# Optimization experiments

Measured on AMD Instinct MI355X. Metric: run time of the kernel, lower is better.

Reference implementation:

```python
import jax, jax.numpy as jnp
import numpy as np

D_MODEL = 1024
N_HEAD = 16
D_HEAD = 64


def setup_inputs() -> dict:
    key = jax.random.key(0)
    k1, k2, k3 = jax.random.split(key, 3)
    B, T = 2, 2048
    x = jax.random.normal(k1, (B, T, D_MODEL), dtype=jnp.float32)
    # Linear weights (scaled like typical init to keep softmax numerics sane)
    w_attn = jax.random.normal(k2, (D_MODEL, 3 * D_MODEL), dtype=jnp.float32) * (1.0 / np.sqrt(D_MODEL))
    w_proj = jax.random.normal(k3, (D_MODEL, D_MODEL), dtype=jnp.float32) * (1.0 / np.sqrt(D_MODEL))
    return {"x": x, "w_attn": w_attn, "w_proj": w_proj}


def reference(x, w_attn, w_proj):
    B, T, C = x.shape
    # c_attn: fused qkv projection (use_bias=False)
    qkv = jnp.einsum('btc,cf->btf', x, w_attn)  # [B, T, 3C]
    q, k, v = jnp.split(qkv, 3, axis=-1)
    q = q.reshape(B, T, N_HEAD, D_HEAD)
    k = k.reshape(B, T, N_HEAD, D_HEAD)
    v = v.reshape(B, T, N_HEAD, D_HEAD)
    # scaled QK^T with causal mask (cache=None training path)
    att = jnp.einsum('bqhd,bkhd->bhqk', q, k) * (1.0 / jnp.sqrt(jnp.float32(D_HEAD)))
    causal = jnp.tril(jnp.ones((T, T), dtype=bool))  # [T, T]
    att = jnp.where(causal[None, None, :, :], att, -jnp.inf)
    att = jax.nn.softmax(att, axis=-1)
    # dropout is a no-op (deterministic / p=0)
    y = jnp.einsum('bhqk,bkhd->bqhd', att, v).reshape(B, T, C)
    y = jnp.einsum('btc,cd->btd', y, w_proj)
    return y
```

## Files before the change

kernel.cpp:

```cpp
#include <hip/hip_runtime.h>
#include <hip/hip_bf16.h>


typedef __attribute__((ext_vector_type(8))) __bf16 bf16x8;
typedef __attribute__((ext_vector_type(4))) float  floatx4;
typedef __attribute__((ext_vector_type(4))) float  fvec4;
typedef __attribute__((ext_vector_type(4))) short  short4v;

#define MFMA16(a, b, c) __builtin_amdgcn_mfma_f32_16x16x32_bf16(a, b, c, 0, 0, 0)

using as1v = const __attribute__((address_space(1))) void;
using as3v = __attribute__((address_space(3))) void;
__device__ __forceinline__ void async16(const void* g, void* l) {
  __builtin_amdgcn_global_load_lds((as1v*)g, (as3v*)l, 16, 0, 0);
}

__global__ __launch_bounds__(256) void prep_kernel(const float* __restrict__ x,
                                                   const float* __restrict__ w_attn,
                                                   const float* __restrict__ w_proj,
                                                   __hip_bfloat16* __restrict__ xb,
                                                   __hip_bfloat16* __restrict__ wat,
                                                   __hip_bfloat16* __restrict__ wpt) {
  const int bid = blockIdx.x, tid = threadIdx.x;
  if (bid < 4096) {
    const int i = (bid * 256 + tid) * 4;
    fvec4 v = *(const fvec4*)(x + i);
    union { short4v s; __hip_bfloat16 h[4]; } u;
#pragma unroll
    for (int j = 0; j < 4; ++j) u.h[j] = __float2bfloat16(v[j]);
    *(short4v*)((short*)xb + i) = u.s;
    return;
  }
  __shared__ __align__(16) __hip_bfloat16 tile[64 * 64];
  const float* in;
  __hip_bfloat16* out;
  int cols, bx, by;
  if (bid < 4864) {
    const int b2 = bid - 4096;
    in = w_attn; out = wat; cols = 3072; bx = b2 % 48; by = b2 / 48;
  } else {
    const int b2 = bid - 4864;
    in = w_proj; out = wpt; cols = 1024; bx = b2 % 16; by = b2 / 16;
  }
  const int c0 = bx * 64, r0 = by * 64;
#pragma unroll
  for (int it = 0; it < 2; ++it) {
    const int c = it * 256 + tid;
    const int row = c >> 3, cg = c & 7;
    const float* src = in + (long)(r0 + row) * cols + c0 + cg * 8;
    fvec4 v0 = *(const fvec4*)src;
    fvec4 v1 = *(const fvec4*)(src + 4);
    union { bf16x8 v; __hip_bfloat16 h[8]; } u;
#pragma unroll
    for (int j = 0; j < 4; ++j) { u.h[j] = __float2bfloat16(v0[j]); u.h[4 + j] = __float2bfloat16(v1[j]); }
    *(bf16x8*)(tile + row * 64 + (cg ^ ((row >> 3) & 7)) * 8) = u.v;
  }
  __syncthreads();
#pragma unroll
  for (int it = 0; it < 2; ++it) {
    const int c = it * 256 + tid;
    const int dr = c >> 3, tg = c & 7;
    union { bf16x8 v; __hip_bfloat16 e[8]; } u;
    const int pg = (dr >> 3) ^ tg;
#pragma unroll
    for (int j = 0; j < 8; ++j)
      u.e[j] = tile[(tg * 8 + j) * 64 + pg * 8 + (dr & 7)];
    *(bf16x8*)(out + (long)(c0 + dr) * 1024 + r0 + tg * 8) = u.v;
  }
}

__global__ __launch_bounds__(256) void gemm_qkv_kernel(const __hip_bfloat16* __restrict__ A,
                                                       const __hip_bfloat16* __restrict__ Bt,
                                                       __hip_bfloat16* __restrict__ qk,
                                                       __hip_bfloat16* __restrict__ vt,
                                                       float qscale) {
  const int K = 1024;
  __shared__ __align__(16) __hip_bfloat16 As[2][128 * 32];
  __shared__ __align__(16) __hip_bfloat16 Bs[2][128 * 32];
  const int tid = threadIdx.x;
  const int lane = tid & 63, wv = tid >> 6;
  const int l15 = lane & 15, quad = lane >> 4;
  const int wm = wv >> 1, wn = wv & 1;
  const long m0 = (long)blockIdx.y * 128, n0 = (long)blockIdx.x * 128;
  floatx4 acc[4][4] = {};
  const int nk = K >> 5;

  auto issue = [&](int kt, int p) {
    const int k0 = kt << 5;
#pragma unroll
    for (int it = 0; it < 2; ++it) {
      const int c = it * 256 + tid;
      const int row = c >> 2;
      const int lcg = (c & 3) ^ ((row >> 1) & 3);
      async16(A + (m0 + row) * K + k0 + lcg * 8, (char*)&As[p][0] + c * 16);
      async16(Bt + (n0 + row) * K + k0 + lcg * 8, (char*)&Bs[p][0] + c * 16);
    }
  };

  issue(0, 0);
  for (int kt = 0; kt < nk; ++kt) {
    const int p = kt & 1;
    __syncthreads();
    if (kt + 1 < nk) issue(kt + 1, p ^ 1);
    bf16x8 af[4], bfr[4];
#pragma unroll
    for (int t = 0; t < 4; ++t) {
      const int ar = wm * 64 + t * 16 + l15;
      const int br = wn * 64 + t * 16 + l15;
      af[t]  = *(const bf16x8*)(&As[p][ar * 32 + (quad ^ ((ar >> 1) & 3)) * 8]);
      bfr[t] = *(const bf16x8*)(&Bs[p][br * 32 + (quad ^ ((br >> 1) & 3)) * 8]);
    }
#pragma unroll
    for (int mt = 0; mt < 4; ++mt)
#pragma unroll
      for (int nt = 0; nt < 4; ++nt)
        acc[mt][nt] = MFMA16(af[mt], bfr[nt], acc[mt][nt]);
  }

#pragma unroll
  for (int nt = 0; nt < 4; ++nt) {
    const int colb = (int)n0 + wn * 64 + nt * 16;
    if (colb >= 2048) {
      const int hh = (colb - 2048) >> 6;
      const int d  = (colb & 63) + l15;
#pragma unroll
      for (int mt = 0; mt < 4; ++mt) {
        const long row = m0 + wm * 64 + mt * 16 + quad * 4;
        const long b   = row >> 11;
        const long t0  = row & 2047;
        union { short4v s; __hip_bfloat16 h[4]; } uy;
#pragma unroll
        for (int r = 0; r < 4; ++r) uy.h[r] = __float2bfloat16(acc[mt][nt][r]);
        *(short4v*)(vt + ((b * 16 + hh) * 64 + d) * 2048 + t0) = uy.s;
      }
    } else {
      const float sc = (colb < 1024) ? qscale : 1.0f;
      const long col = colb + l15;
#pragma unroll
      for (int mt = 0; mt < 4; ++mt)
#pragma unroll
        for (int r = 0; r < 4; ++r) {
          const long row = m0 + wm * 64 + mt * 16 + quad * 4 + r;
          qk[row * 2048 + col] = __float2bfloat16(acc[mt][nt][r] * sc);
        }
    }
  }
}

__global__ __launch_bounds__(256) void gemm_bt128_kernel(const __hip_bfloat16* __restrict__ A,
                                                         const __hip_bfloat16* __restrict__ Bt,
                                                         float* __restrict__ C,
                                                         int M, int N, int K) {
  __shared__ __align__(16) __hip_bfloat16 As[2][128 * 32];
  __shared__ __align__(16) __hip_bfloat16 Bs[2][128 * 32];
  const int tid = threadIdx.x;
  const int lane = tid & 63, wv = tid >> 6;
  const int l15 = lane & 15, quad = lane >> 4;
  const int wm = wv >> 1, wn = wv & 1;
  const long m0 = (long)blockIdx.y * 128, n0 = (long)blockIdx.x * 128;
  floatx4 acc[4][4] = {};
  const int nk = K >> 5;

  auto issue = [&](int kt, int p) {
    const int k0 = kt << 5;
#pragma unroll
    for (int it = 0; it < 2; ++it) {
      const int c = it * 256 + tid;
      const int row = c >> 2;
      const int lcg = (c & 3) ^ ((row >> 1) & 3);
      async16(A + (m0 + row) * K + k0 + lcg * 8, (char*)&As[p][0] + c * 16);
      async16(Bt + (n0 + row) * K + k0 + lcg * 8, (char*)&Bs[p][0] + c * 16);
    }
  };

  issue(0, 0);
  for (int kt = 0; kt < nk; ++kt) {
    const int p = kt & 1;
    __syncthreads();
    if (kt + 1 < nk) issue(kt + 1, p ^ 1);
    bf16x8 af[4], bfr[4];
#pragma unroll
    for (int t = 0; t < 4; ++t) {
      const int ar = wm * 64 + t * 16 + l15;
      const int br = wn * 64 + t * 16 + l15;
      af[t]  = *(const bf16x8*)(&As[p][ar * 32 + (quad ^ ((ar >> 1) & 3)) * 8]);
      bfr[t] = *(const bf16x8*)(&Bs[p][br * 32 + (quad ^ ((br >> 1) & 3)) * 8]);
    }
#pragma unroll
    for (int mt = 0; mt < 4; ++mt)
#pragma unroll
      for (int nt = 0; nt < 4; ++nt)
        acc[mt][nt] = MFMA16(af[mt], bfr[nt], acc[mt][nt]);
  }
#pragma unroll
  for (int mt = 0; mt < 4; ++mt)
#pragma unroll
    for (int nt = 0; nt < 4; ++nt)
#pragma unroll
      for (int r = 0; r < 4; ++r) {
        const long row = m0 + wm * 64 + mt * 16 + quad * 4 + r;
        const long col = n0 + wn * 64 + nt * 16 + l15;
        C[row * N + col] = acc[mt][nt][r];
      }
}

__global__ __launch_bounds__(512, 2) void attn_kernel(const __hip_bfloat16* __restrict__ qk,
                                                      const __hip_bfloat16* __restrict__ vtg,
                                                      __hip_bfloat16* __restrict__ y) {
  __shared__ __align__(16) char smem[81920];
  __hip_bfloat16* KsB = (__hip_bfloat16*)smem;
  __hip_bfloat16* VtB = (__hip_bfloat16*)(smem + 32768);
  __hip_bfloat16* PbB = (__hip_bfloat16*)(smem + 65536);

  const int tid = threadIdx.x;
  const int lane = tid & 63, wv = tid >> 6;
  const int l15 = lane & 15, quad = lane >> 4;
  const int g = wv >> 2, sub = wv & 3;
  const int wg = blockIdx.x;
  const int xcd = wg & 7;
  const int r_ = wg >> 3;
  const int pt = r_ & 15;
  const int hb = xcd + 8 * (r_ >> 4);
  const int h = hb & 15, b = hb >> 4;
  const int qtA = pt, qtB = 31 - pt;
  const int q0A = qtA * 64, q0B = qtB * 64;
  const long bh = (long)b * 16 + h;
  const long RS = 2048;

  const int srow = tid >> 3;
  const int scg = (tid & 7) ^ (srow & 7);
  const __hip_bfloat16* kbase = qk + ((long)b * 2048 + srow) * RS + 1024 + h * 64 + scg * 8;
  const __hip_bfloat16* vbase = vtg + (bh * 64 + srow) * 2048 + scg * 8;
  char* ldst = smem + tid * 16;

  auto issue = [&](int pr, int buf) {
#pragma unroll
    for (int par = 0; par < 2; ++par) {
      const int kt = 2 * pr + par;
      if (kt <= qtB) {
        const long kb = (long)kt * 64;
        async16(kbase + kb * RS, ldst + buf * 16384 + par * 8192);
        async16(vbase + kb,      ldst + 32768 + buf * 16384 + par * 8192);
      }
    }
  };

  bf16x8 bqA0, bqA1, bqB0, bqB1;
  {
    const __hip_bfloat16* qpA = qk + ((long)b * 2048 + q0A + sub * 16 + l15) * RS + h * 64 + quad * 8;
    bqA0 = *(const bf16x8*)qpA;
    bqA1 = *(const bf16x8*)(qpA + 32);
    const __hip_bfloat16* qpB = qk + ((long)b * 2048 + q0B + sub * 16 + l15) * RS + h * 64 + quad * 8;
    bqB0 = *(const bf16x8*)qpB;
    bqB1 = *(const bf16x8*)(qpB + 32);
  }
  union { bf16x8 v; __hip_bfloat16 e[8]; } uo;
#pragma unroll
  for (int j = 0; j < 8; ++j) uo.e[j] = __float2bfloat16(1.0f);
  const bf16x8 ones = uo.v;

  floatx4 oA[4] = {}, oB[4] = {}, o4A = {}, o4B = {};
  __hip_bfloat16* Pw = PbB + wv * (16 * 64);
  const int m7 = l15 & 7;

  const int npairs = (qtB + 2) >> 1;
  issue(0, 0);
  for (int pr = 0; pr < npairs; ++pr) {
    const int buf = pr & 1;
    __syncthreads();
    if (pr + 1 < npairs) issue(pr + 1, buf ^ 1);
    const int kt = 2 * pr + g;
    if (kt > qtB) continue;
    const int kb = kt * 64;
    const __hip_bfloat16* Ksp = KsB + buf * 8192 + g * 4096;
    const __hip_bfloat16* Vsp = VtB + buf * 8192 + g * 4096;

    bf16x8 kf[4][2], vf[4][2];
#pragma unroll
    for (int nt = 0; nt < 4; ++nt) {
      const int row = nt * 16 + l15;
      const int s0 = (quad ^ (row & 7)) * 8, s1 = ((quad + 4) ^ (row & 7)) * 8;
      kf[nt][0] = *(const bf16x8*)(Ksp + row * 64 + s0);
      kf[nt][1] = *(const bf16x8*)(Ksp + row * 64 + s1);
      vf[nt][0] = *(const bf16x8*)(Vsp + row * 64 + s0);
      vf[nt][1] = *(const bf16x8*)(Vsp + row * 64 + s1);
    }

    auto tile = [&](const bf16x8& bq0, const bf16x8& bq1, floatx4* o, floatx4& o4,
                    bool diag, int q0X) {
      floatx4 st[4] = {};
#pragma unroll
      for (int nt = 0; nt < 4; ++nt) {
        st[nt] = MFMA16(kf[nt][0], bq0, st[nt]);
        st[nt] = MFMA16(kf[nt][1], bq1, st[nt]);
      }
      if (diag) {
        const int qg = q0X + sub * 16 + l15;
#pragma unroll
        for (int nt = 0; nt < 4; ++nt) {
          union { short4v s; __hip_bfloat16 h[4]; } up;
#pragma unroll
          for (int r = 0; r < 4; ++r) {
            float pv = exp2f(st[nt][r]);
            if (kb + nt * 16 + quad * 4 + r > qg) pv = 0.f;
            up.h[r] = __float2bfloat16(pv);
          }
          const int chunk = (nt * 2 + (quad >> 1)) ^ m7;
          *(short4v*)(Pw + l15 * 64 + chunk * 8 + (quad & 1) * 4) = up.s;
        }
      } else {
#pragma unroll
        for (int nt = 0; nt < 4; ++nt) {
          union { short4v s; __hip_bfloat16 h[4]; } up;
#pragma unroll
          for (int r = 0; r < 4; ++r) up.h[r] = __float2bfloat16(exp2f(st[nt][r]));
          const int chunk = (nt * 2 + (quad >> 1)) ^ m7;
          *(short4v*)(Pw + l15 * 64 + chunk * 8 + (quad & 1) * 4) = up.s;
        }
      }
      const bf16x8 pb0 = *(const bf16x8*)(Pw + l15 * 64 + (quad ^ m7) * 8);
      const bf16x8 pb1 = *(const bf16x8*)(Pw + l15 * 64 + ((quad + 4) ^ m7) * 8);
#pragma unroll
      for (int mt = 0; mt < 4; ++mt) {
        o[mt] = MFMA16(vf[mt][0], pb0, o[mt]);
        o[mt] = MFMA16(vf[mt][1], pb1, o[mt]);
      }
      o4 = MFMA16(ones, pb0, o4);
      o4 = MFMA16(ones, pb1, o4);
    };

    tile(bqB0, bqB1, oB, o4B, kt == qtB, q0B);
    if (kt <= qtA) tile(bqA0, bqA1, oA, o4A, kt == qtA, q0A);
  }

  __syncthreads();
  floatx4* redv = (floatx4*)smem;
  if (g == 1) {
#pragma unroll
    for (int mt = 0; mt < 4; ++mt) {
      redv[(sub * 10 + mt) * 64 + lane] = oA[mt];
      redv[(sub * 10 + 4 + mt) * 64 + lane] = oB[mt];
    }
    redv[(sub * 10 + 8) * 64 + lane] = o4A;
    redv[(sub * 10 + 9) * 64 + lane] = o4B;
  }
  __syncthreads();
  if (g == 0) {
#pragma unroll
    for (int mt = 0; mt < 4; ++mt) {
      oA[mt] += redv[(sub * 10 + mt) * 64 + lane];
      oB[mt] += redv[(sub * 10 + 4 + mt) * 64 + lane];
    }
    o4A += redv[(sub * 10 + 8) * 64 + lane];
    o4B += redv[(sub * 10 + 9) * 64 + lane];

    auto epi = [&](floatx4* o, floatx4& o4, int q0X) {
      const float inv = 1.0f / o4[0];
      const long t = (long)b * 2048 + q0X + sub * 16 + l15;
#pragma unroll
      for (int mt = 0; mt < 4; ++mt) {
        union { short4v s; __hip_bfloat16 h[4]; } uy;
#pragma unroll
        for (int r = 0; r < 4; ++r) uy.h[r] = __float2bfloat16(o[mt][r] * inv);
        *(short4v*)(y + t * 1024 + h * 64 + mt * 16 + quad * 4) = uy.s;
      }
    };
    epi(oA, o4A, q0A);
    epi(oB, o4B, q0B);
  }
}

extern "C" void kernel_launch(void* const* d_in, const int* in_sizes, int n_in,
                              void* d_out, int out_size, void* d_ws, size_t ws_size,
                              hipStream_t stream) {
  const float* x      = (const float*)d_in[0];
  const float* w_attn = (const float*)d_in[1];
  const float* w_proj = (const float*)d_in[2];
  float* out = (float*)d_out;
  char* ws = (char*)d_ws;
  __hip_bfloat16* xb  = (__hip_bfloat16*)(ws);
  __hip_bfloat16* wat = (__hip_bfloat16*)(ws + 8388608);
  __hip_bfloat16* qk  = (__hip_bfloat16*)(ws + 16777216);
  __hip_bfloat16* wpt = (__hip_bfloat16*)(ws + 33554432);
  __hip_bfloat16* vtg = (__hip_bfloat16*)(ws + 35651584);
  __hip_bfloat16* yb  = wat;
  const float SC = 0.18033688011112042f;

  prep_kernel<<<5120, 256, 0, stream>>>(x, w_attn, w_proj, xb, wat, wpt);
  gemm_qkv_kernel<<<dim3(24, 32), 256, 0, stream>>>(xb, wat, qk, vtg, SC);
  attn_kernel<<<512, 512, 0, stream>>>(qk, vtg, yb);
  gemm_bt128_kernel<<<dim3(8, 32), 256, 0, stream>>>(yb, wpt, out, 4096, 1024, 1024);
}
```

Baseline: 182.1 us.

## Compute softmax row sums in fp32 and interleave the two query tiles' stages

Drops the extra MFMA with an all-ones operand that produced the softmax denominator. Each lane now accumulates the exp values in fp32 and the partial sums are combined with cross-lane shuffles and an LDS reduction. The per-tile lambda is also split up so the QK MFMAs for tile A are issued while tile B's probabilities are written to LDS, and the V fragment loads are deferred. This removes two MFMAs per tile and gives more room for overlap, but it adds VALU adds, shuffles and some register pressure. The denominator now comes from unrounded fp32 values rather than the bf16-rounded ones.

```diff
diff --git a/kernel.cpp b/kernel.cpp
--- a/kernel.cpp
+++ b/kernel.cpp
@@ -254,12 +254,9 @@
     bqB0 = *(const bf16x8*)qpB;
     bqB1 = *(const bf16x8*)(qpB + 32);
   }
-  union { bf16x8 v; __hip_bfloat16 e[8]; } uo;
-#pragma unroll
-  for (int j = 0; j < 8; ++j) uo.e[j] = __float2bfloat16(1.0f);
-  const bf16x8 ones = uo.v;
-
-  floatx4 oA[4] = {}, oB[4] = {}, o4A = {}, o4B = {};
+
+  floatx4 oA[4] = {}, oB[4] = {};
+  float dsA = 0.f, dsB = 0.f;
   __hip_bfloat16* Pw = PbB + wv * (16 * 64);
   const int m7 = l15 & 7;
 
@@ -272,101 +269,139 @@
     const int kt = 2 * pr + g;
     if (kt > qtB) continue;
     const int kb = kt * 64;
+    const bool actA = (kt <= qtA);
     const __hip_bfloat16* Ksp = KsB + buf * 8192 + g * 4096;
     const __hip_bfloat16* Vsp = VtB + buf * 8192 + g * 4096;
 
-    bf16x8 kf[4][2], vf[4][2];
+    auto storeP = [&](floatx4* st, bool diag, int q0X, float& ds) {
+      if (diag) {
+        const int qg = q0X + sub * 16 + l15;
+#pragma unroll
+        for (int nt = 0; nt < 4; ++nt) {
+          union { short4v s; __hip_bfloat16 h2[4]; } up;
+#pragma unroll
+          for (int r = 0; r < 4; ++r) {
+            float pv = exp2f(st[nt][r]);
+            if (kb + nt * 16 + quad * 4 + r > qg) pv = 0.f;
+            ds += pv;
+            up.h2[r] = __float2bfloat16(pv);
+          }
+          const int chunk = (nt * 2 + (quad >> 1)) ^ m7;
+          *(short4v*)(Pw + l15 * 64 + chunk * 8 + (quad & 1) * 4) = up.s;
+        }
+      } else {
+#pragma unroll
+        for (int nt = 0; nt < 4; ++nt) {
+          union { short4v s; __hip_bfloat16 h2[4]; } up;
+#pragma unroll
+          for (int r = 0; r < 4; ++r) {
+            float pv = exp2f(st[nt][r]);
+            ds += pv;
+            up.h2[r] = __float2bfloat16(pv);
+          }
+          const int chunk = (nt * 2 + (quad >> 1)) ^ m7;
+          *(short4v*)(Pw + l15 * 64 + chunk * 8 + (quad & 1) * 4) = up.s;
+        }
+      }
+    };
+
+    bf16x8 kf[4][2];
 #pragma unroll
     for (int nt = 0; nt < 4; ++nt) {
       const int row = nt * 16 + l15;
       const int s0 = (quad ^ (row & 7)) * 8, s1 = ((quad + 4) ^ (row & 7)) * 8;
       kf[nt][0] = *(const bf16x8*)(Ksp + row * 64 + s0);
       kf[nt][1] = *(const bf16x8*)(Ksp + row * 64 + s1);
+    }
+
+    floatx4 st[4] = {};
+#pragma unroll
+    for (int nt = 0; nt < 4; ++nt) {
+      st[nt] = MFMA16(kf[nt][0], bqB0, st[nt]);
+      st[nt] = MFMA16(kf[nt][1], bqB1, st[nt]);
+    }
+    storeP(st, kt == qtB, q0B, dsB);
+
+    if (actA) {
+#pragma unroll
+      for (int nt = 0; nt < 4; ++nt) {
+        floatx4 z = {};
+        z = MFMA16(kf[nt][0], bqA0, z);
+        z = MFMA16(kf[nt][1], bqA1, z);
+        st[nt] = z;
+      }
+    }
+    const bf16x8 pbB0 = *(const bf16x8*)(Pw + l15 * 64 + (quad ^ m7) * 8);
+    const bf16x8 pbB1 = *(const bf16x8*)(Pw + l15 * 64 + ((quad + 4) ^ m7) * 8);
+    if (actA) storeP(st, kt == qtA, q0A, dsA);
+
+    bf16x8 vf[4][2];
+#pragma unroll
+    for (int nt = 0; nt < 4; ++nt) {
+      const int row = nt * 16 + l15;
+      const int s0 = (quad ^ (row & 7)) * 8, s1 = ((quad + 4) ^ (row & 7)) * 8;
       vf[nt][0] = *(const bf16x8*)(Vsp + row * 64 + s0);
       vf[nt][1] = *(const bf16x8*)(Vsp + row * 64 + s1);
     }
-
-    auto tile = [&](const bf16x8& bq0, const bf16x8& bq1, floatx4* o, floatx4& o4,
-                    bool diag, int q0X) {
-      floatx4 st[4] = {};
-#pragma unroll
-      for (int nt = 0; nt < 4; ++nt) {
-        st[nt] = MFMA16(kf[nt][0], bq0, st[nt]);
-        st[nt] = MFMA16(kf[nt][1], bq1, st[nt]);
-      }
-      if (diag) {
-        const int qg = q0X + sub * 16 + l15;
-#pragma unroll
-        for (int nt = 0; nt < 4; ++nt) {
-          union { short4v s; __hip_bfloat16 h[4]; } up;
-#pragma unroll
-          for (int r = 0; r < 4; ++r) {
-            float pv = exp2f(st[nt][r]);
-            if (kb + nt * 16 + quad * 4 + r > qg) pv = 0.f;
-            up.h[r] = __float2bfloat16(pv);
-          }
-          const int chunk = (nt * 2 + (quad >> 1)) ^ m7;
-          *(short4v*)(Pw + l15 * 64 + chunk * 8 + (quad & 1) * 4) = up.s;
-        }
-      } else {
-#pragma unroll
-        for (int nt = 0; nt < 4; ++nt) {
-          union { short4v s; __hip_bfloat16 h[4]; } up;
-#pragma unroll
-          for (int r = 0; r < 4; ++r) up.h[r] = __float2bfloat16(exp2f(st[nt][r]));
-          const int chunk = (nt * 2 + (quad >> 1)) ^ m7;
-          *(short4v*)(Pw + l15 * 64 + chunk * 8 + (quad & 1) * 4) = up.s;
-        }
-      }
-      const bf16x8 pb0 = *(const bf16x8*)(Pw + l15 * 64 + (quad ^ m7) * 8);
-      const bf16x8 pb1 = *(const bf16x8*)(Pw + l15 * 64 + ((quad + 4) ^ m7) * 8);
+    bf16x8 pbA0 = pbB0, pbA1 = pbB1;
+    if (actA) {
+      pbA0 = *(const bf16x8*)(Pw + l15 * 64 + (quad ^ m7) * 8);
+      pbA1 = *(const bf16x8*)(Pw + l15 * 64 + ((quad + 4) ^ m7) * 8);
+    }
+#pragma unroll
+    for (int mt = 0; mt < 4; ++mt) {
+      oB[mt] = MFMA16(vf[mt][0], pbB0, oB[mt]);
+      oB[mt] = MFMA16(vf[mt][1], pbB1, oB[mt]);
+    }
+    if (actA) {
 #pragma unroll
       for (int mt = 0; mt < 4; ++mt) {
-        o[mt] = MFMA16(vf[mt][0], pb0, o[mt]);
-        o[mt] = MFMA16(vf[mt][1], pb1, o[mt]);
-      }
-      o4 = MFMA16(ones, pb0, o4);
-      o4 = MFMA16(ones, pb1, o4);
-    };
-
-    tile(bqB0, bqB1, oB, o4B, kt == qtB, q0B);
-    if (kt <= qtA) tile(bqA0, bqA1, oA, o4A, kt == qtA, q0A);
-  }
+        oA[mt] = MFMA16(vf[mt][0], pbA0, oA[mt]);
+        oA[mt] = MFMA16(vf[mt][1], pbA1, oA[mt]);
+      }
+    }
+  }
+
+  dsA += __shfl_xor(dsA, 16, 64);
+  dsA += __shfl_xor(dsA, 32, 64);
+  dsB += __shfl_xor(dsB, 16, 64);
+  dsB += __shfl_xor(dsB, 32, 64);
 
   __syncthreads();
   floatx4* redv = (floatx4*)smem;
+  float*   redd = (float*)(smem + 32768);
   if (g == 1) {
 #pragma unroll
     for (int mt = 0; mt < 4; ++mt) {
-      redv[(sub * 10 + mt) * 64 + lane] = oA[mt];
-      redv[(sub * 10 + 4 + mt) * 64 + lane] = oB[mt];
-    }
-    redv[(sub * 10 + 8) * 64 + lane] = o4A;
-    redv[(sub * 10 + 9) * 64 + lane] = o4B;
+      redv[(sub * 8 + mt) * 64 + lane] = oA[mt];
+      redv[(sub * 8 + 4 + mt) * 64 + lane] = oB[mt];
+    }
+    redd[(sub * 2 + 0) * 64 + lane] = dsA;
+    redd[(sub * 2 + 1) * 64 + lane] = dsB;
   }
   __syncthreads();
   if (g == 0) {
 #pragma unroll
     for (int mt = 0; mt < 4; ++mt) {
-      oA[mt] += redv[(sub * 10 + mt) * 64 + lane];
-      oB[mt] += redv[(sub * 10 + 4 + mt) * 64 + lane];
-    }
-    o4A += redv[(sub * 10 + 8) * 64 + lane];
-    o4B += redv[(sub * 10 + 9) * 64 + lane];
-
-    auto epi = [&](floatx4* o, floatx4& o4, int q0X) {
-      const float inv = 1.0f / o4[0];
+      oA[mt] += redv[(sub * 8 + mt) * 64 + lane];
+      oB[mt] += redv[(sub * 8 + 4 + mt) * 64 + lane];
+    }
+    dsA += redd[(sub * 2 + 0) * 64 + lane];
+    dsB += redd[(sub * 2 + 1) * 64 + lane];
+
+    auto epi = [&](floatx4* o, float ds, int q0X) {
+      const float inv = 1.0f / ds;
       const long t = (long)b * 2048 + q0X + sub * 16 + l15;
 #pragma unroll
       for (int mt = 0; mt < 4; ++mt) {
-        union { short4v s; __hip_bfloat16 h[4]; } uy;
-#pragma unroll
-        for (int r = 0; r < 4; ++r) uy.h[r] = __float2bfloat16(o[mt][r] * inv);
+        union { short4v s; __hip_bfloat16 h2[4]; } uy;
+#pragma unroll
+        for (int r = 0; r < 4; ++r) uy.h2[r] = __float2bfloat16(o[mt][r] * inv);
         *(short4v*)(y + t * 1024 + h * 64 + mt * 16 + quad * 4) = uy.s;
       }
     };
-    epi(oA, o4A, q0A);
-    epi(oB, o4B, q0B);
+    epi(oA, dsA, q0A);
+    epi(oB, dsB, q0B);
   }
 }
 
```

Measured after the change: 184.6 us. No clear change (+1.4%).

## Load K/V directly from global per wave, drop LDS staging and split-K reduction

Applied to the files above, without the earlier changes.

The attention kernel no longer stages K and V tiles through double-buffered LDS with async loads. Each wave now reads its K and V fragments straight from global memory, and the two wave groups each own one query tile instead of splitting keys and reducing through shared memory. The softmax denominator now comes from a shuffle-reduced scalar sum rather than extra MFMAs against a ones vector. This removes barriers, the reduction pass and LDS traffic, but K/V reuse across waves now depends on cache hits, and waves in the same block do unbalanced amounts of work (pt versus 31-pt tiles).

```diff
diff --git a/kernel.cpp b/kernel.cpp
--- a/kernel.cpp
+++ b/kernel.cpp
@@ -207,166 +207,112 @@
 __global__ __launch_bounds__(512, 2) void attn_kernel(const __hip_bfloat16* __restrict__ qk,
                                                       const __hip_bfloat16* __restrict__ vtg,
                                                       __hip_bfloat16* __restrict__ y) {
-  __shared__ __align__(16) char smem[81920];
-  __hip_bfloat16* KsB = (__hip_bfloat16*)smem;
-  __hip_bfloat16* VtB = (__hip_bfloat16*)(smem + 32768);
-  __hip_bfloat16* PbB = (__hip_bfloat16*)(smem + 65536);
+  __shared__ __align__(16) __hip_bfloat16 Pb[8][16 * 64];
 
   const int tid = threadIdx.x;
   const int lane = tid & 63, wv = tid >> 6;
   const int l15 = lane & 15, quad = lane >> 4;
-  const int g = wv >> 2, sub = wv & 3;
+  const int sub = wv & 3;
   const int wg = blockIdx.x;
   const int xcd = wg & 7;
   const int r_ = wg >> 3;
   const int pt = r_ & 15;
   const int hb = xcd + 8 * (r_ >> 4);
   const int h = hb & 15, b = hb >> 4;
-  const int qtA = pt, qtB = 31 - pt;
-  const int q0A = qtA * 64, q0B = qtB * 64;
+  const int qt = (wv >> 2) ? (31 - pt) : pt;
+  const int q0 = qt * 64;
   const long bh = (long)b * 16 + h;
   const long RS = 2048;
 
-  const int srow = tid >> 3;
-  const int scg = (tid & 7) ^ (srow & 7);
-  const __hip_bfloat16* kbase = qk + ((long)b * 2048 + srow) * RS + 1024 + h * 64 + scg * 8;
-  const __hip_bfloat16* vbase = vtg + (bh * 64 + srow) * 2048 + scg * 8;
-  char* ldst = smem + tid * 16;
-
-  auto issue = [&](int pr, int buf) {
-#pragma unroll
-    for (int par = 0; par < 2; ++par) {
-      const int kt = 2 * pr + par;
-      if (kt <= qtB) {
-        const long kb = (long)kt * 64;
-        async16(kbase + kb * RS, ldst + buf * 16384 + par * 8192);
-        async16(vbase + kb,      ldst + 32768 + buf * 16384 + par * 8192);
+  bf16x8 bq0, bq1;
+  {
+    const __hip_bfloat16* qp = qk + ((long)b * 2048 + q0 + sub * 16 + l15) * RS + h * 64 + quad * 8;
+    bq0 = *(const bf16x8*)qp;
+    bq1 = *(const bf16x8*)(qp + 32);
+  }
+
+  const __hip_bfloat16* kp[4];
+  const __hip_bfloat16* vp[4];
+#pragma unroll
+  for (int nt = 0; nt < 4; ++nt) {
+    kp[nt] = qk + ((long)b * 2048 + nt * 16 + l15) * RS + 1024 + h * 64 + quad * 8;
+    vp[nt] = vtg + (bh * 64 + nt * 16 + l15) * RS + quad * 8;
+  }
+
+  floatx4 o[4] = {};
+  float ds = 0.f;
+  __hip_bfloat16* Pw = &Pb[wv][0];
+  const int m7 = l15 & 7;
+
+  for (int kt = 0; kt <= qt; ++kt) {
+    const int kb = kt * 64;
+    const long koff = (long)kb * RS;
+    bf16x8 fr[4][2];
+#pragma unroll
+    for (int nt = 0; nt < 4; ++nt) {
+      fr[nt][0] = *(const bf16x8*)(kp[nt] + koff);
+      fr[nt][1] = *(const bf16x8*)(kp[nt] + koff + 32);
+    }
+    floatx4 st[4] = {};
+#pragma unroll
+    for (int nt = 0; nt < 4; ++nt) {
+      st[nt] = MFMA16(fr[nt][0], bq0, st[nt]);
+      st[nt] = MFMA16(fr[nt][1], bq1, st[nt]);
+    }
+    if (kt == qt) {
+      const int qg = q0 + sub * 16 + l15;
+#pragma unroll
+      for (int nt = 0; nt < 4; ++nt) {
+        union { short4v s; __hip_bfloat16 h2[4]; } up;
+#pragma unroll
+        for (int r = 0; r < 4; ++r) {
+          float pv = exp2f(st[nt][r]);
+          if (kb + nt * 16 + quad * 4 + r > qg) pv = 0.f;
+          ds += pv;
+          up.h2[r] = __float2bfloat16(pv);
+        }
+        const int chunk = (nt * 2 + (quad >> 1)) ^ m7;
+        *(short4v*)(Pw + l15 * 64 + chunk * 8 + (quad & 1) * 4) = up.s;
       }
-    }
-  };
-
-  bf16x8 bqA0, bqA1, bqB0, bqB1;
-  {
-    const __hip_bfloat16* qpA = qk + ((long)b * 2048 + q0A + sub * 16 + l15) * RS + h * 64 + quad * 8;
-    bqA0 = *(const bf16x8*)qpA;
-    bqA1 = *(const bf16x8*)(qpA + 32);
-    const __hip_bfloat16* qpB = qk + ((long)b * 2048 + q0B + sub * 16 + l15) * RS + h * 64 + quad * 8;
-    bqB0 = *(const bf16x8*)qpB;
-    bqB1 = *(const bf16x8*)(qpB + 32);
-  }
-  union { bf16x8 v; __hip_bfloat16 e[8]; } uo;
-#pragma unroll
-  for (int j = 0; j < 8; ++j) uo.e[j] = __float2bfloat16(1.0f);
-  const bf16x8 ones = uo.v;
-
-  floatx4 oA[4] = {}, oB[4] = {}, o4A = {}, o4B = {};
-  __hip_bfloat16* Pw = PbB + wv * (16 * 64);
-  const int m7 = l15 & 7;
-
-  const int npairs = (qtB + 2) >> 1;
-  issue(0, 0);
-  for (int pr = 0; pr < npairs; ++pr) {
-    const int buf = pr & 1;
-    __syncthreads();
-    if (pr + 1 < npairs) issue(pr + 1, buf ^ 1);
-    const int kt = 2 * pr + g;
-    if (kt > qtB) continue;
-    const int kb = kt * 64;
-    const __hip_bfloat16* Ksp = KsB + buf * 8192 + g * 4096;
-    const __hip_bfloat16* Vsp = VtB + buf * 8192 + g * 4096;
-
-    bf16x8 kf[4][2], vf[4][2];
+    } else {
+#pragma unroll
+      for (int nt = 0; nt < 4; ++nt) {
+        union { short4v s; __hip_bfloat16 h2[4]; } up;
+#pragma unroll
+        for (int r = 0; r < 4; ++r) {
+          float pv = exp2f(st[nt][r]);
+          ds += pv;
+          up.h2[r] = __float2bfloat16(pv);
+        }
+        const int chunk = (nt * 2 + (quad >> 1)) ^ m7;
+        *(short4v*)(Pw + l15 * 64 + chunk * 8 + (quad & 1) * 4) = up.s;
+      }
+    }
+    const bf16x8 pb0 = *(const bf16x8*)(Pw + l15 * 64 + (quad ^ m7) * 8);
+    const bf16x8 pb1 = *(const bf16x8*)(Pw + l15 * 64 + ((quad + 4) ^ m7) * 8);
 #pragma unroll
     for (int nt = 0; nt < 4; ++nt) {
-      const int row = nt * 16 + l15;
-      const int s0 = (quad ^ (row & 7)) * 8, s1 = ((quad + 4) ^ (row & 7)) * 8;
-      kf[nt][0] = *(const bf16x8*)(Ksp + row * 64 + s0);
-      kf[nt][1] = *(const bf16x8*)(Ksp + row * 64 + s1);
-      vf[nt][0] = *(const bf16x8*)(Vsp + row * 64 + s0);
-      vf[nt][1] = *(const bf16x8*)(Vsp + row * 64 + s1);
-    }
-
-    auto tile = [&](const bf16x8& bq0, const bf16x8& bq1, floatx4* o, floatx4& o4,
-                    bool diag, int q0X) {
-      floatx4 st[4] = {};
-#pragma unroll
-      for (int nt = 0; nt < 4; ++nt) {
-        st[nt] = MFMA16(kf[nt][0], bq0, st[nt]);
-        st[nt] = MFMA16(kf[nt][1], bq1, st[nt]);
-      }
-      if (diag) {
-        const int qg = q0X + sub * 16 + l15;
-#pragma unroll
-        for (int nt = 0; nt < 4; ++nt) {
-          union { short4v s; __hip_bfloat16 h[4]; } up;
-#pragma unroll
-          for (int r = 0; r < 4; ++r) {
-            float pv = exp2f(st[nt][r]);
-            if (kb + nt * 16 + quad * 4 + r > qg) pv = 0.f;
-            up.h[r] = __float2bfloat16(pv);
-          }
-          const int chunk = (nt * 2 + (quad >> 1)) ^ m7;
-          *(short4v*)(Pw + l15 * 64 + chunk * 8 + (quad & 1) * 4) = up.s;
-        }
-      } else {
-#pragma unroll
-        for (int nt = 0; nt < 4; ++nt) {
-          union { short4v s; __hip_bfloat16 h[4]; } up;
-#pragma unroll
-          for (int r = 0; r < 4; ++r) up.h[r] = __float2bfloat16(exp2f(st[nt][r]));
-          const int chunk = (nt * 2 + (quad >> 1)) ^ m7;
-          *(short4v*)(Pw + l15 * 64 + chunk * 8 + (quad & 1) * 4) = up.s;
-        }
-      }
-      const bf16x8 pb0 = *(const bf16x8*)(Pw + l15 * 64 + (quad ^ m7) * 8);
-      const bf16x8 pb1 = *(const bf16x8*)(Pw + l15 * 64 + ((quad + 4) ^ m7) * 8);
-#pragma unroll
-      for (int mt = 0; mt < 4; ++mt) {
-        o[mt] = MFMA16(vf[mt][0], pb0, o[mt]);
-        o[mt] = MFMA16(vf[mt][1], pb1, o[mt]);
-      }
-      o4 = MFMA16(ones, pb0, o4);
-      o4 = MFMA16(ones, pb1, o4);
-    };
-
-    tile(bqB0, bqB1, oB, o4B, kt == qtB, q0B);
-    if (kt <= qtA) tile(bqA0, bqA1, oA, o4A, kt == qtA, q0A);
-  }
-
-  __syncthreads();
-  floatx4* redv = (floatx4*)smem;
-  if (g == 1) {
+      fr[nt][0] = *(const bf16x8*)(vp[nt] + kb);
+      fr[nt][1] = *(const bf16x8*)(vp[nt] + kb + 32);
+    }
 #pragma unroll
     for (int mt = 0; mt < 4; ++mt) {
-      redv[(sub * 10 + mt) * 64 + lane] = oA[mt];
-      redv[(sub * 10 + 4 + mt) * 64 + lane] = oB[mt];
-    }
-    redv[(sub * 10 + 8) * 64 + lane] = o4A;
-    redv[(sub * 10 + 9) * 64 + lane] = o4B;
-  }
-  __syncthreads();
-  if (g == 0) {
-#pragma unroll
-    for (int mt = 0; mt < 4; ++mt) {
-      oA[mt] += redv[(sub * 10 + mt) * 64 + lane];
-      oB[mt] += redv[(sub * 10 + 4 + mt) * 64 + lane];
-    }
-    o4A += redv[(sub * 10 + 8) * 64 + lane];
-    o4B += redv[(sub * 10 + 9) * 64 + lane];
-
-    auto epi = [&](floatx4* o, floatx4& o4, int q0X) {
-      const float inv = 1.0f / o4[0];
-      const long t = (long)b * 2048 + q0X + sub * 16 + l15;
-#pragma unroll
-      for (int mt = 0; mt < 4; ++mt) {
-        union { short4v s; __hip_bfloat16 h[4]; } uy;
-#pragma unroll
-        for (int r = 0; r < 4; ++r) uy.h[r] = __float2bfloat16(o[mt][r] * inv);
-        *(short4v*)(y + t * 1024 + h * 64 + mt * 16 + quad * 4) = uy.s;
-      }
-    };
-    epi(oA, o4A, q0A);
-    epi(oB, o4B, q0B);
+      o[mt] = MFMA16(fr[mt][0], pb0, o[mt]);
+      o[mt] = MFMA16(fr[mt][1], pb1, o[mt]);
+    }
+  }
+
+  ds += __shfl_xor(ds, 16, 64);
+  ds += __shfl_xor(ds, 32, 64);
+  const float inv = 1.0f / ds;
+
+  const long t = (long)b * 2048 + q0 + sub * 16 + l15;
+#pragma unroll
+  for (int mt = 0; mt < 4; ++mt) {
+    union { short4v s; __hip_bfloat16 h2[4]; } uy;
+#pragma unroll
+    for (int r = 0; r < 4; ++r) uy.h2[r] = __float2bfloat16(o[mt][r] * inv);
+    *(short4v*)(y + t * 1024 + h * 64 + mt * 16 + quad * 4) = uy.s;
   }
 }
 
```

Measured after the change: 258.3 us. 1.42x slower.
